# Kernel optimization log

Measured on AMD Instinct MI355X. Metric: run time of the kernel, lower is better.

The kernel has to match this reference:

```python
import jax, jax.numpy as jnp
import numpy as np

TABLE_SIZE = 256
I16_MIN, I16_MAX = -32768.0, 32767.0
I8_MIN, I8_MAX = -128.0, 127.0
MAX_SOFTMAX_VALUE = 1.0
OUT_SCALE = MAX_SOFTMAX_VALUE * 2.0 / 255.0            # int8 output scale
EXP_OUT_SCALE = 2.0 / 65535.0                          # qint16 exp output scale
RECIP_OUT_SCALE = (1.0 / 0.1) * 2.0 / 65535.0          # qint16 reciprocal output scale
# (xmin, xmax, kind) in ascending x order; 'table' = 256-entry LUT, 'line' = linear fit
EXP_REGIONS = [(-40.0, -20.0, 'line'), (-20.0, -10.0, 'table'), (-10.0, 0.0, 'table'), (0.0, 1.0, 'line')]
RECIP_REGIONS = [(0.001, 0.1, 'line'), (0.1, 250.0, 'table'), (250.0, 500.0, 'table'), (500.0, 700.0, 'line')]


def _quant(y, out_scale, qmin, qmax):
    return jnp.clip(jnp.round(y / out_scale), qmin, qmax)


def _piecewise(x, func, regions, out_scale, qmin, qmax):
    """Piecewise quantized approximation of func: constant / line / 256-entry
    table regions, returning quantized (integer-valued float) outputs."""
    left_c = _quant(func(jnp.float32(regions[0][0])), out_scale, qmin, qmax)
    y = left_c * jnp.ones_like(x)
    for xmin, xmax, kind in regions:
        if kind == 'table':
            xs = jnp.linspace(xmin, xmax, TABLE_SIZE)
            tab = _quant(func(xs), out_scale, qmin, qmax)
            idx = jnp.clip(jnp.round((x - xmin) * ((TABLE_SIZE - 1) / (xmax - xmin))), 0, TABLE_SIZE - 1).astype(jnp.int32)
            y_r = tab[idx]
        else:
            y0 = func(jnp.float32(xmin))
            y1 = func(jnp.float32(xmax))
            y_r = _quant(y0 + (x - xmin) * ((y1 - y0) / (xmax - xmin)), out_scale, qmin, qmax)
        y = jnp.where(x >= xmin, y_r, y)
    right_c = _quant(func(jnp.float32(regions[-1][1])), out_scale, qmin, qmax)
    return jnp.where(x > regions[-1][1], right_c, y)


def setup_inputs() -> dict:
    key = jax.random.key(0)
    k1, _ = jax.random.split(key)
    data = jax.random.randint(k1, (32, 128, 80, 80), -128, 128, dtype=jnp.int32)  # int8 repr, zp=0
    data_scale = jnp.array([0.0625], dtype=jnp.float32)
    return {"data": data, "data_scale": data_scale}


def reference(data, data_scale):
    ds = data_scale[0]
    C = data.shape[1]
    shift = float(np.ceil(np.log2(C)))  # rescale_shift for the exp-sum
    # max-subtract in the integer domain, dequantize diff (zero_point = 0)
    qmax = jnp.max(data, axis=1, keepdims=True)
    xd = (data - qmax).astype(jnp.float32) * ds  # [B,C,H,W], in (-inf, 0]
    # quantized exp via piecewise tables -> qint16 with EXP_OUT_SCALE
    exp_q = _piecewise(xd, jnp.exp, EXP_REGIONS, EXP_OUT_SCALE, I16_MIN, I16_MAX)
    # sum over channels, right-shift back into int16 range
    sum_q = jnp.sum(exp_q, axis=1, keepdims=True)
    sum_sh = jnp.clip(jnp.round(sum_q * (2.0 ** -shift)), I16_MIN, I16_MAX)
    div_scale = EXP_OUT_SCALE * (2.0 ** shift)  # div_data_scale
    # quantized reciprocal of the (dequantized) shifted sum -> qint16
    recip_q = _piecewise(sum_sh * div_scale, lambda v: 1.0 / v, RECIP_REGIONS, RECIP_OUT_SCALE, I16_MIN, I16_MAX)
    # out = exp * recip, requantized to int8 with OUT_SCALE, then dequantized
    out_q = jnp.clip(jnp.round(exp_q * recip_q * (EXP_OUT_SCALE * RECIP_OUT_SCALE / OUT_SCALE)), I8_MIN, I8_MAX)
    return out_q * OUT_SCALE
```

## Files before the change

kernel.cpp:

```cpp
#include <hip/hip_runtime.h>
#include <cmath>

#define NB  32
#define NC  128
#define NHW 6400
#define TPB 64

typedef float vfloat4 __attribute__((ext_vector_type(4)));

__global__ __launch_bounds__(64) void lut_build_kernel(
    int* __restrict__ exp_ws, float* __restrict__ rec_ws,
    const float* __restrict__ dscale) {
#pragma clang fp contract(off)
  const int t = blockIdx.x * 64 + threadIdx.x;
  const float ds = dscale[0];

  const float EXP_SCALE_F = (float)(2.0 / 65535.0);
  float x = (float)(-t) * ds;
  float e;
  if (x >= 0.0f) {
    float y0 = expf(0.0f), y1 = expf(1.0f);
    e = rintf((y0 + x * ((y1 - y0) / 1.0f)) / EXP_SCALE_F);
  } else if (x >= -10.0f) {
    float delta = 10.0f / 255.0f;
    float idxf = rintf((x + 10.0f) * 25.5f);
    idxf = fminf(fmaxf(idxf, 0.0f), 255.0f);
    float xs = -10.0f + idxf * delta;
    e = rintf((float)exp((double)xs) / EXP_SCALE_F);
  } else {
    float delta = 10.0f / 255.0f;
    float idxf = rintf((x + 20.0f) * 25.5f);
    idxf = fminf(fmaxf(idxf, 0.0f), 255.0f);
    float xs = -20.0f + idxf * delta;
    e = rintf((float)exp((double)xs) / EXP_SCALE_F);
  }
  e = fminf(fmaxf(e, -32768.0f), 32767.0f);
  exp_ws[t] = (int)e;

  const float RECIP_SCALE_F = (float)((1.0 / 0.1) * 2.0 / 65535.0);
  float deltar = (250.0f - 0.1f) / 255.0f;
  float xs = 0.1f + (float)t * deltar;
  float r = rintf((1.0f / xs) / RECIP_SCALE_F);
  r = fminf(fmaxf(r, -32768.0f), 32767.0f);
  rec_ws[t] = r;
}

__global__ __launch_bounds__(TPB) void qsoftmax_kernel(
    const int* __restrict__ data,
    const int* __restrict__ exp_ws,
    const float* __restrict__ rec_ws,
    float* __restrict__ out) {
#pragma clang fp contract(off)
  __shared__ int   exp_tab[256];
  __shared__ float recip_tab[256];

  const int t = threadIdx.x;

  {
    int4   ev = ((const int4*)exp_ws)[t];
    float4 rv = ((const float4*)rec_ws)[t];
    ((int4*)exp_tab)[t]     = ev;
    ((float4*)recip_tab)[t] = rv;
  }

  const int blk = blockIdx.x;
  const int b   = blk / (NHW / TPB);
  const int hw  = (blk % (NHW / TPB)) * TPB + t;
  const int* gp = data + b * NC * NHW + hw;

  int m = -128;
#pragma unroll 32
  for (int c = 0; c < NC; ++c) {
    m = max(m, gp[c * NHW]);
  }

  int pe[NC / 2];
  int ssum = 0;
#pragma unroll
  for (int c = 0; c < NC; c += 2) {
    int v0 = gp[c * NHW];
    int v1 = gp[(c + 1) * NHW];
    int e0 = exp_tab[m - v0];
    int e1 = exp_tab[m - v1];
    ssum += e0;
    ssum += e1;
    pe[c >> 1] = e0 | (e1 << 16);
  }

  const float DIV_SCALE_F = (float)((2.0 / 65535.0) * 128.0);
  const float RIDX_K_F    = (float)(255.0 / (250.0 - 0.1));
  float rq;
  {
    float ss = rintf((float)ssum * 0.0078125f);
    ss = fminf(fmaxf(ss, -32768.0f), 32767.0f);
    float v = ss * DIV_SCALE_F;
    float idxf = rintf((v - 0.1f) * RIDX_K_F);
    idxf = fminf(fmaxf(idxf, 0.0f), 255.0f);
    rq = recip_tab[(int)idxf];
  }

  const float K_F = (float)((2.0 / 65535.0) * ((1.0 / 0.1) * 2.0 / 65535.0) / (2.0 / 255.0));
  const float OUT_SCALE_F = (float)(2.0 / 255.0);
  float* op = out + b * NC * NHW + hw;
#pragma unroll
  for (int c = 0; c < NC; c += 2) {
    int p = pe[c >> 1];
    float e0 = (float)(p & 0xFFFF);
    float e1 = (float)((unsigned)p >> 16);
    float o0 = fminf(fmaxf(rintf((e0 * rq) * K_F), -128.0f), 127.0f) * OUT_SCALE_F;
    float o1 = fminf(fmaxf(rintf((e1 * rq) * K_F), -128.0f), 127.0f) * OUT_SCALE_F;
    __builtin_nontemporal_store(o0, &op[c * NHW]);
    __builtin_nontemporal_store(o1, &op[(c + 1) * NHW]);
  }
}

extern "C" void kernel_launch(void* const* d_in, const int* in_sizes, int n_in,
                              void* d_out, int out_size, void* d_ws, size_t ws_size,
                              hipStream_t stream) {
  const int* data     = (const int*)d_in[0];
  const float* dscale = (const float*)d_in[1];
  float* out          = (float*)d_out;
  (void)in_sizes; (void)n_in; (void)out_size; (void)ws_size;

  int*   exp_ws = (int*)d_ws;
  float* rec_ws = (float*)((char*)d_ws + 1024);

  lut_build_kernel<<<dim3(4), dim3(64), 0, stream>>>(exp_ws, rec_ws, dscale);
  qsoftmax_kernel<<<dim3(NB * (NHW / TPB)), dim3(TPB), 0, stream>>>(
      data, exp_ws, rec_ws, out);
}
```

Before: 204.1 us.

## Load input once with int4 vectors, stage packed bytes in LDS, split channels across warps

```diff
diff --git a/kernel.cpp b/kernel.cpp
--- a/kernel.cpp
+++ b/kernel.cpp
@@ -1,10 +1,11 @@
 #include <hip/hip_runtime.h>
 #include <cmath>
 
-#define NB  32
-#define NC  128
-#define NHW 6400
-#define TPB 64
+#define NB   32
+#define NC   128
+#define NHW  6400
+#define TILE 256
+#define TPB  256
 
 typedef float vfloat4 __attribute__((ext_vector_type(4)));
 
@@ -51,66 +52,111 @@
     const float* __restrict__ rec_ws,
     float* __restrict__ out) {
 #pragma clang fp contract(off)
-  __shared__ int   exp_tab[256];
-  __shared__ float recip_tab[256];
+  __shared__ unsigned int lds_data[NC * 64];
+  __shared__ int          exp_tab[256];
+  __shared__ float        recip_tab[256];
+  __shared__ unsigned int red_mp[4 * 64];
+  __shared__ int4         red_s[4][64];
 
   const int t = threadIdx.x;
+  const int w = t >> 6;
+  const int l = t & 63;
 
-  {
-    int4   ev = ((const int4*)exp_ws)[t];
-    float4 rv = ((const float4*)rec_ws)[t];
-    ((int4*)exp_tab)[t]     = ev;
-    ((float4*)recip_tab)[t] = rv;
+  const int blk  = blockIdx.x;
+  const int b    = blk / (NHW / TILE);
+  const int hw0  = (blk % (NHW / TILE)) * TILE;
+  const int base4 = b * NC * (NHW / 4) + (hw0 >> 2) + l;
+
+  exp_tab[t]   = exp_ws[t];
+  recip_tab[t] = rec_ws[t];
+
+  const int4* g4 = (const int4*)data;
+  int4 m = make_int4(-128, -128, -128, -128);
+#pragma unroll 8
+  for (int j = 0; j < 32; ++j) {
+    const int c = w + 4 * j;
+    int4 v = g4[base4 + c * (NHW / 4)];
+    m.x = max(m.x, v.x); m.y = max(m.y, v.y);
+    m.z = max(m.z, v.z); m.w = max(m.w, v.w);
+    lds_data[c * 64 + l] = (unsigned)((v.x & 255) | ((v.y & 255) << 8) |
+                                      ((v.z & 255) << 16) |
+                                      ((unsigned)(v.w & 255) << 24));
+  }
+  red_mp[w * 64 + l] = (unsigned)((m.x & 255) | ((m.y & 255) << 8) |
+                                  ((m.z & 255) << 16) |
+                                  ((unsigned)(m.w & 255) << 24));
+  __syncthreads();
+
+  int4 q = make_int4(-128, -128, -128, -128);
+#pragma unroll
+  for (int ww = 0; ww < 4; ++ww) {
+    unsigned mp = red_mp[ww * 64 + l];
+    q.x = max(q.x, (int)(signed char)(mp));
+    q.y = max(q.y, (int)(signed char)(mp >> 8));
+    q.z = max(q.z, (int)(signed char)(mp >> 16));
+    q.w = max(q.w, (int)(signed char)(mp >> 24));
   }
 
-  const int blk = blockIdx.x;
-  const int b   = blk / (NHW / TPB);
-  const int hw  = (blk % (NHW / TPB)) * TPB + t;
-  const int* gp = data + b * NC * NHW + hw;
+  int4 s = make_int4(0, 0, 0, 0);
+#pragma unroll 8
+  for (int j = 0; j < 32; ++j) {
+    const int c = w + 4 * j;
+    unsigned pdv = lds_data[c * 64 + l];
+    int c0 = (int)(signed char)(pdv);
+    int c1 = (int)(signed char)(pdv >> 8);
+    int c2 = (int)(signed char)(pdv >> 16);
+    int c3 = (int)(signed char)(pdv >> 24);
+    s.x += exp_tab[q.x - c0];
+    s.y += exp_tab[q.y - c1];
+    s.z += exp_tab[q.z - c2];
+    s.w += exp_tab[q.w - c3];
+  }
+  red_s[w][l] = s;
+  __syncthreads();
 
-  int m = -128;
-#pragma unroll 32
-  for (int c = 0; c < NC; ++c) {
-    m = max(m, gp[c * NHW]);
+  int4 tot = red_s[0][l];
+#pragma unroll
+  for (int ww = 1; ww < 4; ++ww) {
+    int4 r = red_s[ww][l];
+    tot.x += r.x; tot.y += r.y; tot.z += r.z; tot.w += r.w;
   }
-
-  int pe[NC / 2];
-  int ssum = 0;
-#pragma unroll
-  for (int c = 0; c < NC; c += 2) {
-    int v0 = gp[c * NHW];
-    int v1 = gp[(c + 1) * NHW];
-    int e0 = exp_tab[m - v0];
-    int e1 = exp_tab[m - v1];
-    ssum += e0;
-    ssum += e1;
-    pe[c >> 1] = e0 | (e1 << 16);
-  }
-
   const float DIV_SCALE_F = (float)((2.0 / 65535.0) * 128.0);
   const float RIDX_K_F    = (float)(255.0 / (250.0 - 0.1));
-  float rq;
+  float rq[4];
   {
-    float ss = rintf((float)ssum * 0.0078125f);
-    ss = fminf(fmaxf(ss, -32768.0f), 32767.0f);
-    float v = ss * DIV_SCALE_F;
-    float idxf = rintf((v - 0.1f) * RIDX_K_F);
-    idxf = fminf(fmaxf(idxf, 0.0f), 255.0f);
-    rq = recip_tab[(int)idxf];
+    int tv[4] = {tot.x, tot.y, tot.z, tot.w};
+#pragma unroll
+    for (int jj = 0; jj < 4; ++jj) {
+      float ss = rintf((float)tv[jj] * 0.0078125f);
+      ss = fminf(fmaxf(ss, -32768.0f), 32767.0f);
+      float v = ss * DIV_SCALE_F;
+      float idxf = rintf((v - 0.1f) * RIDX_K_F);
+      idxf = fminf(fmaxf(idxf, 0.0f), 255.0f);
+      rq[jj] = recip_tab[(int)idxf];
+    }
   }
 
   const float K_F = (float)((2.0 / 65535.0) * ((1.0 / 0.1) * 2.0 / 65535.0) / (2.0 / 255.0));
   const float OUT_SCALE_F = (float)(2.0 / 255.0);
-  float* op = out + b * NC * NHW + hw;
-#pragma unroll
-  for (int c = 0; c < NC; c += 2) {
-    int p = pe[c >> 1];
-    float e0 = (float)(p & 0xFFFF);
-    float e1 = (float)((unsigned)p >> 16);
-    float o0 = fminf(fmaxf(rintf((e0 * rq) * K_F), -128.0f), 127.0f) * OUT_SCALE_F;
-    float o1 = fminf(fmaxf(rintf((e1 * rq) * K_F), -128.0f), 127.0f) * OUT_SCALE_F;
-    __builtin_nontemporal_store(o0, &op[c * NHW]);
-    __builtin_nontemporal_store(o1, &op[(c + 1) * NHW]);
+  vfloat4* o4 = (vfloat4*)out;
+#pragma unroll 8
+  for (int j = 0; j < 32; ++j) {
+    const int c = w + 4 * j;
+    unsigned pdv = lds_data[c * 64 + l];
+    int c0 = (int)(signed char)(pdv);
+    int c1 = (int)(signed char)(pdv >> 8);
+    int c2 = (int)(signed char)(pdv >> 16);
+    int c3 = (int)(signed char)(pdv >> 24);
+    float e0 = (float)exp_tab[q.x - c0];
+    float e1 = (float)exp_tab[q.y - c1];
+    float e2 = (float)exp_tab[q.z - c2];
+    float e3 = (float)exp_tab[q.w - c3];
+    vfloat4 o;
+    o.x = fminf(fmaxf(rintf((e0 * rq[0]) * K_F), -128.0f), 127.0f) * OUT_SCALE_F;
+    o.y = fminf(fmaxf(rintf((e1 * rq[1]) * K_F), -128.0f), 127.0f) * OUT_SCALE_F;
+    o.z = fminf(fmaxf(rintf((e2 * rq[2]) * K_F), -128.0f), 127.0f) * OUT_SCALE_F;
+    o.w = fminf(fmaxf(rintf((e3 * rq[3]) * K_F), -128.0f), 127.0f) * OUT_SCALE_F;
+    __builtin_nontemporal_store(o, &o4[base4 + c * (NHW / 4)]);
   }
 }
 
@@ -126,6 +172,6 @@
   float* rec_ws = (float*)((char*)d_ws + 1024);
 
   lut_build_kernel<<<dim3(4), dim3(64), 0, stream>>>(exp_ws, rec_ws, dscale);
-  qsoftmax_kernel<<<dim3(NB * (NHW / TPB)), dim3(TPB), 0, stream>>>(
+  qsoftmax_kernel<<<dim3(NB * (NHW / TILE)), dim3(TPB), 0, stream>>>(
       data, exp_ws, rec_ws, out);
 }
```

Measured after the change: 196.4 us. 1.04x faster.
